# Performance work log

Measured on AMD Instinct MI355X. Metric: run time of the kernel, lower is better.

The kernel has to match this reference:

```python
import jax, jax.numpy as jnp
import numpy as np

D_STATE = 64
D_CONV = 5
HEADDIM = 64
EXPAND = 2


def setup_inputs() -> dict:
    key = jax.random.key(0)
    ks = jax.random.split(key, 12)
    b, ch, h, w = 4, 128, 64, 64
    d_inner = EXPAND * ch
    nheads = d_inner // HEADDIM
    conv_ch = d_inner + 2 * D_STATE
    d_in_proj = 2 * d_inner + 2 * D_STATE + nheads
    s = lambda k, shape, scale: jax.random.normal(k, shape, jnp.float32) * scale
    return {
        "noisy": s(ks[0], (b, ch, h, w), 1.0),
        "aux": s(ks[1], (b, ch, h, w), 1.0),
        "ln_gamma": jnp.ones((ch,), jnp.float32),
        "ln_beta": jnp.zeros((ch,), jnp.float32),
        "in_proj_w": s(ks[2], (d_in_proj, ch), ch ** -0.5),
        "conv_w": s(ks[3], (conv_ch, D_CONV), D_CONV ** -0.5),
        "conv_b": s(ks[4], (conv_ch,), 0.02),
        "A_log": jnp.log(jnp.linspace(1.0, 16.0, nheads)).astype(jnp.float32),
        "dt_bias": s(ks[5], (nheads,), 0.1),
        "D": jnp.ones((nheads,), jnp.float32),
        "rms_w": jnp.ones((d_inner,), jnp.float32),
        "out_proj_w": s(ks[6], (ch, d_inner), d_inner ** -0.5),
        "ff_w1": s(ks[7], (ch, ch, 3, 3), (ch * 9) ** -0.5),
        "ff_b1": jnp.zeros((ch,), jnp.float32),
        "ff_w2": s(ks[8], (ch, ch, 3, 3), (ch * 9) ** -0.5),
        "ff_b2": jnp.zeros((ch,), jnp.float32),
    }


def _mamba2(u, in_proj_w, conv_w, conv_b, A_log, dt_bias, D_skip, rms_w, out_proj_w):
    # u: (b, L, d_model). Mamba2 with ngroups=1, headdim=64.
    b, L, d = u.shape
    d_inner = EXPAND * d
    nheads = d_inner // HEADDIM
    zxbcdt = u @ in_proj_w.T  # (b, L, 2*d_inner + 2*d_state + nheads)
    z = zxbcdt[..., :d_inner]
    xBC = zxbcdt[..., d_inner:2 * d_inner + 2 * D_STATE]
    dt = jax.nn.softplus(zxbcdt[..., -nheads:] + dt_bias)  # (b, L, h)
    # causal depthwise conv1d along L + SiLU
    xBC_c = jnp.transpose(xBC, (0, 2, 1))  # (b, C, L)
    xBC_c = jax.lax.conv_general_dilated(
        xBC_c, conv_w[:, None, :], (1,), [(D_CONV - 1, 0)],
        feature_group_count=xBC_c.shape[1])
    xBC = jax.nn.silu(jnp.transpose(xBC_c + conv_b[None, :, None], (0, 2, 1)))
    x = xBC[..., :d_inner]
    B = xBC[..., d_inner:d_inner + D_STATE]  # (b, L, n)
    C = xBC[..., d_inner + D_STATE:]         # (b, L, n)
    A = -jnp.exp(A_log)                      # (h,)
    xh = x.reshape(b, L, nheads, HEADDIM)    # (b, L, h, p)
    dA = jnp.exp(dt * A)                     # (b, L, h)

    def step(hstate, inputs):
        dA_t, dt_t, x_t, B_t, C_t = inputs
        hstate = hstate * dA_t[:, :, None, None] + jnp.einsum('bh,bhp,bn->bhpn', dt_t, x_t, B_t)
        y_t = jnp.einsum('bhpn,bn->bhp', hstate, C_t)
        return hstate, y_t

    init = jnp.zeros((b, nheads, HEADDIM, D_STATE), u.dtype)
    xs = (jnp.moveaxis(dA, 1, 0), jnp.moveaxis(dt, 1, 0), jnp.moveaxis(xh, 1, 0),
          jnp.moveaxis(B, 1, 0), jnp.moveaxis(C, 1, 0))
    _, ys = jax.lax.scan(step, init, xs)
    y = jnp.moveaxis(ys, 0, 1) + xh * D_skip[None, None, :, None]  # (b, L, h, p)
    y = y.reshape(b, L, d_inner)
    # gated RMSNorm: rmsnorm(y * silu(z)) * weight
    y = y * jax.nn.silu(z)
    y = y * jax.lax.rsqrt(jnp.mean(y * y, axis=-1, keepdims=True) + 1e-5) * rms_w
    return y @ out_proj_w.T


def _conv3x3_reflect(x, w, b):
    x = jnp.pad(x, ((0, 0), (0, 0), (1, 1), (1, 1)), mode='reflect')
    return jax.lax.conv_general_dilated(x, w, (1, 1), 'VALID') + b[None, :, None, None]


def reference(noisy, aux, ln_gamma, ln_beta, in_proj_w, conv_w, conv_b, A_log,
              dt_bias, D, rms_w, out_proj_w, ff_w1, ff_b1, ff_w2, ff_b2):
    b, c, h, w = noisy.shape
    flat = jnp.transpose(noisy, (0, 2, 3, 1)).reshape(b, h * w, c)
    mu = jnp.mean(flat, axis=-1, keepdims=True)
    var = jnp.var(flat, axis=-1, keepdims=True)
    normed = (flat - mu) * jax.lax.rsqrt(var + 1e-5) * ln_gamma + ln_beta
    m = _mamba2(normed, in_proj_w, conv_w, conv_b, A_log, dt_bias, D, rms_w, out_proj_w)
    m = jnp.transpose(m.reshape(b, h, w, c), (0, 3, 1, 2))
    y = noisy + m
    ff = jax.nn.relu(_conv3x3_reflect(y, ff_w1, ff_b1))
    ff = jax.nn.relu(_conv3x3_reflect(ff, ff_w2, ff_b2))
    y = y + ff
    return (y, aux)
```

## Files before the change

kernel.cpp:

```cpp
#include <hip/hip_runtime.h>
#include <cstddef>

#define B_      4
#define C_      128
#define L_      4096
#define DIN     256
#define NH      4
#define HD      64
#define DS      64
#define CONVCH  384
#define DPROJ   644
#define CHUNK   64
#define NCHUNK  64

typedef short bf16x8 __attribute__((ext_vector_type(8)));
typedef float floatx16 __attribute__((ext_vector_type(16)));

__device__ __forceinline__ float siluf(float v) { return v / (1.f + __expf(-v)); }

__device__ __forceinline__ ushort f2bf(float v) {
  unsigned u = __float_as_uint(v);
  unsigned r = (u + 0x7fff + ((u >> 16) & 1)) >> 16;
  return (ushort)r;
}
__device__ __forceinline__ float bf2f(ushort h) {
  return __uint_as_float((unsigned)h << 16);
}

__device__ __forceinline__ void split8(float4 v0, float4 v1, bf16x8& hi, bf16x8& lo) {
  float f[8] = {v0.x, v0.y, v0.z, v0.w, v1.x, v1.y, v1.z, v1.w};
#pragma unroll
  for (int j = 0; j < 8; ++j) {
    ushort h = f2bf(f[j]);
    hi[j] = (short)h;
    lo[j] = (short)f2bf(f[j] - bf2f(h));
  }
}

__global__ __launch_bounds__(256) void wprep_all(
    const float* __restrict__ ipw, ushort* __restrict__ Bh, ushort* __restrict__ Bl,
    const float* __restrict__ opw, ushort* __restrict__ Oh, ushort* __restrict__ Ol,
    const float* __restrict__ fw1, ushort* __restrict__ Wt1,
    const float* __restrict__ fw2, ushort* __restrict__ Wt2) {
  int bi = blockIdx.x;
  int t = threadIdx.x;
  if (bi < 176) {
    int e = bi * 256 + t;
    int d = e >> 6;
    int c0 = (e & 63) * 2;
    int kk = c0 >> 4;
    int l = (d & 31) + 32 * ((c0 & 15) >> 3);
    int j = c0 & 7;
    size_t off = (((size_t)(d >> 5)) * 8 + kk) * 512 + l * 8 + j;
    float v0 = d < 644 ? ipw[(size_t)d * 128 + c0] : 0.f;
    float v1 = d < 644 ? ipw[(size_t)d * 128 + c0 + 1] : 0.f;
    ushort h0 = f2bf(v0), h1 = f2bf(v1);
    *(unsigned*)(Bh + off) = (unsigned)h0 | ((unsigned)h1 << 16);
    *(unsigned*)(Bl + off) = (unsigned)f2bf(v0 - bf2f(h0)) |
                             ((unsigned)f2bf(v1 - bf2f(h1)) << 16);
  } else if (bi < 304) {
    int e = (bi - 176) * 256 + t;
    int d = e >> 8;
    int c = e & 255;
    size_t f = ((size_t)(d >> 5) * 16 + (c >> 4)) * 512 +
               ((d & 31) + 32 * ((c & 15) >> 3)) * 8 + (c & 7);
    float v = opw[(size_t)d * 256 + c];
    ushort h = f2bf(v);
    Oh[f] = h;
    Ol[f] = f2bf(v - bf2f(h));
  } else {
    const float* fw = bi < 432 ? fw1 : fw2;
    ushort* Wt = bi < 432 ? Wt1 : Wt2;
    int co = (bi - 304) & 127;
    int cb = co >> 5;
    for (int e = t; e < 1152; e += 256) {
      int tap = e >> 7;
      int ci = e & 127;
      int kk = ci >> 4, k16 = ci & 15;
      int l = (co & 31) + 32 * (k16 >> 3);
      int off = ((tap * 8 + kk) * 4 + cb) * 512 + l * 8 + (k16 & 7);
      Wt[off] = f2bf(fw[(size_t)co * 1152 + ci * 9 + tap]);
    }
  }
}

__global__ __launch_bounds__(1024) void ln_gemm1(
    const float* __restrict__ noisy, const float* __restrict__ gamma,
    const float* __restrict__ beta,
    const ushort* __restrict__ Bh, const ushort* __restrict__ Bl,
    float* __restrict__ ZX) {
  int row = blockIdx.x, b = blockIdx.y;
  int t = threadIdx.x;
  __shared__ float tile[64 * 129];
  __shared__ float ps[16][64], pq[16][64];
  __shared__ float smu[64], srs[64];
  __shared__ __align__(16) ushort AhL[8192];
  __shared__ __align__(16) ushort AlL[8192];
  int px = t & 63, cg = t >> 6;
  float s = 0.f, s2 = 0.f;
  const float* src = noisy + ((size_t)b * C_) * L_ + row * 64;
  for (int i = 0; i < 8; ++i) {
    int c = cg * 8 + i;
    float v = src[(size_t)c * L_ + px];
    tile[px * 129 + c] = v;
    s += v; s2 += v * v;
  }
  ps[cg][px] = s; pq[cg][px] = s2;
  __syncthreads();
  if (t < 64) {
    float a = 0.f, qq = 0.f;
#pragma unroll
    for (int g = 0; g < 16; ++g) { a += ps[g][t]; qq += pq[g][t]; }
    float mu = a * (1.f / 128.f);
    float var = qq * (1.f / 128.f) - mu * mu;
    smu[t] = mu;
    srs[t] = rsqrtf(var + 1e-5f);
  }
  __syncthreads();
  for (int idx = t; idx < 4096; idx += 1024) {
    int p2 = idx >> 6;
    int c0 = (idx & 63) * 2;
    float v0 = (tile[p2 * 129 + c0] - smu[p2]) * srs[p2] * gamma[c0] + beta[c0];
    float v1 = (tile[p2 * 129 + c0 + 1] - smu[p2]) * srs[p2] * gamma[c0 + 1] + beta[c0 + 1];
    int kk = c0 >> 4;
    int l = (p2 & 31) + 32 * ((c0 & 15) >> 3);
    int j = c0 & 7;
    int off = ((p2 >> 5) * 8 + kk) * 512 + l * 8 + j;
    ushort h0 = f2bf(v0), h1 = f2bf(v1);
    *(unsigned*)(AhL + off) = (unsigned)h0 | ((unsigned)h1 << 16);
    *(unsigned*)(AlL + off) = (unsigned)f2bf(v0 - bf2f(h0)) |
                              ((unsigned)f2bf(v1 - bf2f(h1)) << 16);
  }
  __syncthreads();
  int wv = t >> 6, lane = t & 63;
  int db = wv & 1, pb = (wv >> 1) & 1, bq = wv >> 2;
  int rowadd = 4 * (lane >> 5);
  for (int bn = bq; bn < 11; bn += 4) {
    floatx16 acc;
#pragma unroll
    for (int i = 0; i < 16; ++i) acc[i] = 0.f;
    size_t bbase = ((size_t)(bn * 2 + db) * 8) * 64 + lane;
    const bf16x8* pBh = (const bf16x8*)Bh + bbase;
    const bf16x8* pBl = (const bf16x8*)Bl + bbase;
#pragma unroll
    for (int kk = 0; kk < 8; ++kk) {
      bf16x8 ah = *(const bf16x8*)(AhL + (pb * 8 + kk) * 512 + lane * 8);
      bf16x8 al = *(const bf16x8*)(AlL + (pb * 8 + kk) * 512 + lane * 8);
      bf16x8 bh = pBh[kk * 64];
      bf16x8 bl = pBl[kk * 64];
      acc = __builtin_amdgcn_mfma_f32_32x32x16_bf16(ah, bh, acc, 0, 0, 0);
      acc = __builtin_amdgcn_mfma_f32_32x32x16_bf16(al, bh, acc, 0, 0, 0);
      acc = __builtin_amdgcn_mfma_f32_32x32x16_bf16(ah, bl, acc, 0, 0, 0);
    }
    int d = bn * 64 + db * 32 + (lane & 31);
    if (d < 644) {
#pragma unroll
      for (int r = 0; r < 16; ++r) {
        int rowm = (r & 3) + 8 * (r >> 2) + rowadd;
        int pix = row * 64 + pb * 32 + rowm;
        ZX[((size_t)(b * L_ + pix)) * DPROJ + d] = acc[r];
      }
    }
  }
}

__global__ __launch_bounds__(384) void conv1d_silu(
    const float* __restrict__ ZX, const float* __restrict__ cw,
    const float* __restrict__ cb, float* __restrict__ XBC) {
  int ch = threadIdx.x;
  int l0 = blockIdx.x * 16, b = blockIdx.y;
  const float* base = ZX + ((size_t)b * L_) * DPROJ + DIN + ch;
  float w0 = cw[ch * 5], w1 = cw[ch * 5 + 1], w2 = cw[ch * 5 + 2],
        w3 = cw[ch * 5 + 3], w4 = cw[ch * 5 + 4];
  float bias = cb[ch];
  float win[20];
#pragma unroll
  for (int i = 0; i < 20; ++i) {
    int ll = l0 - 4 + i;
    win[i] = ll >= 0 ? base[(size_t)ll * DPROJ] : 0.f;
  }
  float* dst = XBC + ((size_t)(b * L_ + l0)) * CONVCH + ch;
#pragma unroll
  for (int j = 0; j < 16; ++j) {
    float acc = bias + w0 * win[j] + w1 * win[j + 1] + w2 * win[j + 2] +
                w3 * win[j + 3] + w4 * win[j + 4];
    dst[(size_t)j * CONVCH] = siluf(acc);
  }
}

#define UPDA(k, B4, C4) \
  st[4*k+0] = st[4*k+0]*da + cf*B4.x; y0 += st[4*k+0]*C4.x; \
  st[4*k+1] = st[4*k+1]*da + cf*B4.y; y1 += st[4*k+1]*C4.y; \
  st[4*k+2] = st[4*k+2]*da + cf*B4.z; y2 += st[4*k+2]*C4.z; \
  st[4*k+3] = st[4*k+3]*da + cf*B4.w; y3 += st[4*k+3]*C4.w;

__global__ __launch_bounds__(256, 4) void scan_passA(
    const float* __restrict__ XBC, const float* __restrict__ ZX,
    const float* __restrict__ dt_bias, const float* __restrict__ A_log,
    float* __restrict__ YL, float* __restrict__ SC, float* __restrict__ PC,
    float* __restrict__ CUM) {
  int chunk = blockIdx.x, h = blockIdx.y, b = blockIdx.z;
  int t = threadIdx.x;
  int p = t >> 2, q = t & 3;
  int bh = b * NH + h;
  __shared__ float sdt[CHUNK], sda[CHUNK];
  __shared__ float sB[32][64];
  __shared__ float sCc[32][64];
  __shared__ float sx[32][64];
  if (t < CHUNK) {
    int l = chunk * CHUNK + t;
    float v = ZX[((size_t)(b * L_ + l)) * DPROJ + 640 + h] + dt_bias[h];
    float dt = v > 20.f ? v : log1pf(expf(v));
    sdt[t] = dt;
    sda[t] = expf(dt * -expf(A_log[h]));
  }
  size_t rowbase = ((size_t)b * L_ + (size_t)chunk * CHUNK) * CONVCH;
  float* __restrict__ yl = YL + ((size_t)b * L_ + (size_t)chunk * CHUNK) * DIN + h * HD + p;
  float* __restrict__ cumout = CUM + (size_t)bh * L_ + chunk * CHUNK;
  float st[16];
#pragma unroll
  for (int j = 0; j < 16; ++j) st[j] = 0.f;
  float cum = 1.f;
  for (int half = 0; half < 2; ++half) {
    __syncthreads();
#pragma unroll
    for (int i = 0; i < 2; ++i) {
      int e = t + i * 256;
      int row = e >> 4, c4 = (e & 15) * 4;
      const float* gsrc = XBC + rowbase + (size_t)(half * 32 + row) * CONVCH;
      *(float4*)&sB[row][c4]  = *(const float4*)(gsrc + DIN + c4);
      *(float4*)&sCc[row][c4] = *(const float4*)(gsrc + DIN + DS + c4);
      *(float4*)&sx[row][c4]  = *(const float4*)(gsrc + h * HD + c4);
    }
    __syncthreads();
#pragma unroll 4
    for (int tl = 0; tl < 32; ++tl) {
      int tg = half * 32 + tl;
      float da = sda[tg], dtv = sdt[tg];
      float x = sx[tl][p];
      float cf = dtv * x;
      const float4* br = (const float4*)&sB[tl][q * 16];
      const float4* cr = (const float4*)&sCc[tl][q * 16];
      float4 B0 = br[0], B1 = br[1], B2 = br[2], B3 = br[3];
      float4 C0 = cr[0], C1 = cr[1], C2 = cr[2], C3 = cr[3];
      float y0 = 0.f, y1 = 0.f, y2 = 0.f, y3 = 0.f;
      UPDA(0, B0, C0) UPDA(1, B1, C1) UPDA(2, B2, C2) UPDA(3, B3, C3)
      float y = (y0 + y1) + (y2 + y3);
      y += __shfl_xor(y, 1);
      y += __shfl_xor(y, 2);
      cum *= da;
      if (q == 0) yl[(size_t)tg * DIN] = y;
      if (t == 0) cumout[tg] = cum;
    }
  }
  float* scp = SC + ((size_t)bh * NCHUNK + chunk) * 4096 + p * 64 + q * 16;
  *(float4*)(scp + 0)  = make_float4(st[0], st[1], st[2], st[3]);
  *(float4*)(scp + 4)  = make_float4(st[4], st[5], st[6], st[7]);
  *(float4*)(scp + 8)  = make_float4(st[8], st[9], st[10], st[11]);
  *(float4*)(scp + 12) = make_float4(st[12], st[13], st[14], st[15]);
  if (t == 0) PC[bh * NCHUNK + chunk] = cum;
}

__global__ __launch_bounds__(256) void scan_passB(
    float* __restrict__ SC, const float* __restrict__ PC) {
  int bh = blockIdx.x >> 4;
  int eg = blockIdx.x & 15;
  int e = eg * 256 + threadIdx.x;
  float h = 0.f;
#pragma unroll 8
  for (int c = 0; c < NCHUNK; ++c) {
    size_t idx = ((size_t)bh * NCHUNK + c) * 4096 + e;
    float s = SC[idx];
    float pcv = PC[bh * NCHUNK + c];
    SC[idx] = h;
    h = h * pcv + s;
  }
}

__global__ __launch_bounds__(1024) void passC_gate(
    const float* __restrict__ XBC, const float* __restrict__ SC,
    const float* __restrict__ CUM, const float* __restrict__ Dp,
    const float* __restrict__ YL, const float* __restrict__ ZX,
    const float* __restrict__ rmsw,
    const ushort* __restrict__ Oh, const ushort* __restrict__ Ol,
    const float* __restrict__ noisy, float* __restrict__ YRES) {
  __shared__ float yt[16384];
  __shared__ __align__(16) ushort fr[32768];
  int chunk = blockIdx.x, b = blockIdx.y;
  int t = threadIdx.x;
  int wv = t >> 6, lane = t & 63;
  size_t pix0g = (size_t)b * L_ + (size_t)chunk * CHUNK;
  float* sCcf  = (float*)fr;
  float* scumf = sCcf + 4096;

  float4 zr[4];
  {
    int lp = t & 31, slot2 = t >> 5;
#pragma unroll
    for (int it = 0; it < 2; ++it) {
      const float* z = ZX + (pix0g + it * 32 + slot2) * DPROJ;
      zr[it * 2]     = *(const float4*)(z + lp * 4);
      zr[it * 2 + 1] = *(const float4*)(z + 128 + lp * 4);
    }
  }
  for (int i = t; i < 4096; i += 1024) {
    *(float4*)&yt[i * 4] = *(const float4*)&YL[pix0g * DIN + (size_t)i * 4];
  }
  {
    int px = t >> 4, slot = t & 15;
    float4 cv = *(const float4*)(XBC + (pix0g + px) * CONVCH + DIN + DS + slot * 4);
    ((float4*)sCcf)[px * 16 + (slot ^ (px & 7))] = cv;
    if (t < 256) {
      int hh = t >> 6, px2 = t & 63;
      scumf[t] = CUM[((size_t)(b * NH + hh)) * L_ + chunk * CHUNK + px2];
    }
  }
  __syncthreads();

  {
    int px = t >> 4, c4 = (t & 15) * 4;
    const float* xs = XBC + (pix0g + px) * CONVCH;
#pragma unroll
    for (int hh = 0; hh < 4; ++hh) {
      float4 xv = *(const float4*)(xs + hh * HD + c4);
      float dv = Dp[hh];
      float* dst = &yt[px * 256 + hh * 64 + c4];
      dst[0] += xv.x * dv; dst[1] += xv.y * dv;
      dst[2] += xv.z * dv; dst[3] += xv.w * dv;
    }
  }
  __syncthreads();

  {
    int h1 = wv >> 2, ptile = (wv >> 1) & 1, pxtile = wv & 1;
    int arow = pxtile * 32 + (lane & 31);
    const float* Sb = SC + (((size_t)(b * NH + h1)) * NCHUNK + chunk) * 4096 +
                      (size_t)(ptile * 32 + (lane & 31)) * 64 + (lane >> 5) * 8;
    const float4* av = (const float4*)sCcf + arow * 16;
    int s0 = (lane >> 5) * 2;
    floatx16 acc;
#pragma unroll
    for (int i = 0; i < 16; ++i) acc[i] = 0.f;
#pragma unroll
    for (int kk = 0; kk < 4; ++kk) {
      float4 b0 = *(const float4*)(Sb + kk * 16);
      float4 b1 = *(const float4*)(Sb + kk * 16 + 4);
      int sa = kk * 4 + s0;
      float4 a0 = av[sa ^ (arow & 7)];
      float4 a1 = av[(sa + 1) ^ (arow & 7)];
      bf16x8 ah, al, bh, bl;
      split8(a0, a1, ah, al);
      split8(b0, b1, bh, bl);
      acc = __builtin_amdgcn_mfma_f32_32x32x16_bf16(ah, bh, acc, 0, 0, 0);
      acc = __builtin_amdgcn_mfma_f32_32x32x16_bf16(al, bh, acc, 0, 0, 0);
      acc = __builtin_amdgcn_mfma_f32_32x32x16_bf16(ah, bl, acc, 0, 0, 0);
    }
    int col = h1 * 64 + ptile * 32 + (lane & 31);
    int radd = 4 * (lane >> 5);
#pragma unroll
    for (int r = 0; r < 16; ++r) {
      int pxl = (r & 3) + 8 * (r >> 2) + radd;
      int px = pxtile * 32 + pxl;
      yt[px * 256 + col] += acc[r] * scumf[h1 * 64 + px];
    }
  }
  __syncthreads();

  ushort* AhL = fr;
  ushort* AlL = fr + 16384;
  {
    int lp = t & 31;
    int slot = t >> 5;
    float4 w0 = *(const float4*)(rmsw + lp * 4);
    float4 w1 = *(const float4*)(rmsw + 128 + lp * 4);
#pragma unroll
    for (int it = 0; it < 2; ++it) {
      int pl = it * 32 + slot;
      const float* y = &yt[pl * 256];
      float4 y0 = *(const float4*)(y + lp * 4);
      float4 y1 = *(const float4*)(y + 128 + lp * 4);
      float4 z0 = zr[it * 2];
      float4 z1 = zr[it * 2 + 1];
      float g[8];
      g[0] = y0.x * siluf(z0.x); g[1] = y0.y * siluf(z0.y);
      g[2] = y0.z * siluf(z0.z); g[3] = y0.w * siluf(z0.w);
      g[4] = y1.x * siluf(z1.x); g[5] = y1.y * siluf(z1.y);
      g[6] = y1.z * siluf(z1.z); g[7] = y1.w * siluf(z1.w);
      float ss = 0.f;
#pragma unroll
      for (int j = 0; j < 8; ++j) ss += g[j] * g[j];
      ss += __shfl_xor(ss, 16);
      ss += __shfl_xor(ss, 8);
      ss += __shfl_xor(ss, 4);
      ss += __shfl_xor(ss, 2);
      ss += __shfl_xor(ss, 1);
      float rs = rsqrtf(ss * (1.f / 256.f) + 1e-5f);
      float o[8];
      o[0] = g[0] * rs * w0.x; o[1] = g[1] * rs * w0.y;
      o[2] = g[2] * rs * w0.z; o[3] = g[3] * rs * w0.w;
      o[4] = g[4] * rs * w1.x; o[5] = g[5] * rs * w1.y;
      o[6] = g[6] * rs * w1.z; o[7] = g[7] * rs * w1.w;
#pragma unroll
      for (int grp = 0; grp < 2; ++grp) {
        int d = grp * 128 + lp * 4;
        int off = ((pl >> 5) * 16 + (d >> 4)) * 512 +
                  ((pl & 31) + 32 * ((d & 15) >> 3)) * 8 + (d & 7);
        ushort h0 = f2bf(o[grp*4+0]), h1 = f2bf(o[grp*4+1]);
        ushort h2 = f2bf(o[grp*4+2]), h3 = f2bf(o[grp*4+3]);
        uint2 hv, lv;
        hv.x = (unsigned)h0 | ((unsigned)h1 << 16);
        hv.y = (unsigned)h2 | ((unsigned)h3 << 16);
        lv.x = (unsigned)f2bf(o[grp*4+0] - bf2f(h0)) | ((unsigned)f2bf(o[grp*4+1] - bf2f(h1)) << 16);
        lv.y = (unsigned)f2bf(o[grp*4+2] - bf2f(h2)) | ((unsigned)f2bf(o[grp*4+3] - bf2f(h3)) << 16);
        *(uint2*)(AhL + off) = hv;
        *(uint2*)(AlL + off) = lv;
      }
    }
  }
  __syncthreads();

  floatx16 acc;
#pragma unroll
  for (int i = 0; i < 16; ++i) acc[i] = 0.f;
  int pb = wv >> 2, bn = (wv >> 1) & 1, db = wv & 1;
  int rowadd = 4 * (lane >> 5);
  if (wv < 8) {
    const bf16x8* pBh = (const bf16x8*)Oh;
    const bf16x8* pBl = (const bf16x8*)Ol;
    size_t bbase = ((size_t)(bn * 2 + db) * 16) * 64 + lane;
#pragma unroll
    for (int kk = 0; kk < 16; ++kk) {
      bf16x8 ah = *(const bf16x8*)(AhL + (pb * 16 + kk) * 512 + lane * 8);
      bf16x8 al = *(const bf16x8*)(AlL + (pb * 16 + kk) * 512 + lane * 8);
      bf16x8 bh = pBh[bbase + (size_t)kk * 64];
      bf16x8 bl = pBl[bbase + (size_t)kk * 64];
      acc = __builtin_amdgcn_mfma_f32_32x32x16_bf16(ah, bh, acc, 0, 0, 0);
      acc = __builtin_amdgcn_mfma_f32_32x32x16_bf16(al, bh, acc, 0, 0, 0);
      acc = __builtin_amdgcn_mfma_f32_32x32x16_bf16(ah, bl, acc, 0, 0, 0);
    }
  } else {
    int t2 = t - 512;
#pragma unroll
    for (int k = 0; k < 16; ++k) {
      int idx = t2 + k * 512;
      int c = idx >> 6, px = idx & 63;
      yt[idx] = noisy[((size_t)(b * C_ + c)) * L_ + chunk * CHUNK + px];
    }
  }
  __syncthreads();

  float* tile = (float*)fr;
  if (wv < 8) {
#pragma unroll
    for (int r = 0; r < 16; ++r) {
      int rowm = (r & 3) + 8 * (r >> 2) + rowadd;
      int rowp = pb * 32 + rowm;
      int col = bn * 64 + db * 32 + (lane & 31);
      tile[rowp * 129 + col] = acc[r];
    }
  }
  __syncthreads();
  for (int idx = t; idx < 8192; idx += 1024) {
    int c = idx >> 6, px = idx & 63;
    size_t o = ((size_t)(b * C_ + c)) * L_ + chunk * CHUNK + px;
    YRES[o] = yt[idx] + tile[px * 129 + c];
  }
}

template <int MODE>
__global__ __launch_bounds__(512) void conv3x3_direct(
    const void* __restrict__ inv, const ushort* __restrict__ Wt,
    const float* __restrict__ bias, const float* __restrict__ res,
    void* __restrict__ outv, const float* __restrict__ aux) {
  int y = blockIdx.x, b = blockIdx.y;
  int t = threadIdx.x;
  if (MODE == 1 && blockIdx.z == 1) {
    const float4* s = (const float4*)aux;
    float4* d = (float4*)((float*)outv + 2097152);
    int base = (b * 64 + y) * 512 + t;
#pragma unroll
    for (int k = 0; k < 4; ++k) d[base + k * 131072] = s[base + k * 131072];
    return;
  }
  __shared__ __align__(16) ushort lds[3 * 64 * 128];
  int lane = t & 63;
  int wv = t >> 6;
  int ry[3];
  ry[0] = y == 0 ? 1 : y - 1;
  ry[1] = y;
  ry[2] = y == 63 ? 62 : y + 1;
  {
    int x = lane;
    for (int u = wv; u < 48; u += 8) {
      int r = u / 16;
      int cib = u % 16;
      int ci0 = cib * 8;
      ushort vals[8];
#pragma unroll
      for (int j = 0; j < 8; ++j) {
        size_t src = ((size_t)(b * C_ + ci0 + j)) * L_ + ry[r] * 64 + x;
        if (MODE == 0) vals[j] = f2bf(((const float*)inv)[src]);
        else           vals[j] = ((const ushort*)inv)[src];
      }
      int idx = (r * 64 + x) * 128 + (cib ^ (x & 15)) * 8;
      *(int4*)&lds[idx] = *(int4*)vals;
    }
  }
  __syncthreads();
  int cb = wv >> 1, nb = wv & 1;
  int n = lane & 31, hi = lane >> 5;
  floatx16 acc0, acc1;
#pragma unroll
  for (int i = 0; i < 16; ++i) { acc0[i] = 0.f; acc1[i] = 0.f; }
  const bf16x8* pW = (const bf16x8*)Wt;
  for (int tap = 0; tap < 9; ++tap) {
    int ky = tap / 3, kx = tap % 3;
    int xg = nb * 32 + n + kx - 1;
    int xx = xg < 0 ? 1 : (xg > 63 ? 62 : xg);
    int base = (ky * 64 + xx) * 128;
    int xs = xx & 15;
#pragma unroll
    for (int kk = 0; kk < 8; ++kk) {
      bf16x8 av = pW[(size_t)((tap * 8 + kk) * 4 + cb) * 64 + lane];
      bf16x8 bv = *(const bf16x8*)&lds[base + ((kk * 2 + hi) ^ xs) * 8];
      if (kk & 1) acc1 = __builtin_amdgcn_mfma_f32_32x32x16_bf16(av, bv, acc1, 0, 0, 0);
      else        acc0 = __builtin_amdgcn_mfma_f32_32x32x16_bf16(av, bv, acc0, 0, 0, 0);
    }
  }
  int x0 = nb * 32 + (lane & 31);
  int rowadd = 4 * (lane >> 5);
#pragma unroll
  for (int r = 0; r < 16; ++r) {
    int rowm = (r & 3) + 8 * (r >> 2) + rowadd;
    int co = cb * 32 + rowm;
    size_t o = ((size_t)(b * C_ + co)) * L_ + y * 64 + x0;
    float v = fmaxf(acc0[r] + acc1[r] + bias[co], 0.f);
    if (MODE == 0) {
      ((ushort*)outv)[o] = f2bf(v);
    } else {
      ((float*)outv)[o] = v + res[o];
    }
  }
}

extern "C" void kernel_launch(void* const* d_in, const int* in_sizes, int n_in,
                              void* d_out, int out_size, void* d_ws, size_t ws_size,
                              hipStream_t stream) {
  const float* noisy   = (const float*)d_in[0];
  const float* aux     = (const float*)d_in[1];
  const float* ln_g    = (const float*)d_in[2];
  const float* ln_b    = (const float*)d_in[3];
  const float* ipw     = (const float*)d_in[4];
  const float* cw      = (const float*)d_in[5];
  const float* cbv     = (const float*)d_in[6];
  const float* A_log   = (const float*)d_in[7];
  const float* dt_bias = (const float*)d_in[8];
  const float* Dp      = (const float*)d_in[9];
  const float* rmsw    = (const float*)d_in[10];
  const float* opw     = (const float*)d_in[11];
  const float* fw1     = (const float*)d_in[12];
  const float* fb1     = (const float*)d_in[13];
  const float* fw2     = (const float*)d_in[14];
  const float* fb2     = (const float*)d_in[15];
  float* out = (float*)d_out;
  float* ws  = (float*)d_ws;

  const size_t OFF_ZX   = 0;
  const size_t OFF_XBC  = OFF_ZX + 16384UL * 644;
  const size_t OFF_SCN  = OFF_XBC + 16384UL * 384;
  const size_t OFF_WT   = OFF_SCN + 4194304UL;
  const size_t OFF_WO   = OFF_WT + 73728UL;
  const size_t OFF_CUM  = OFF_WT + 131072UL;
  const size_t OFF_YL   = OFF_CUM + 65536UL;
  const size_t OFF_PC   = OFF_YL + 16384UL * 256;
  const size_t OFF_WT2  = OFF_PC + 1024UL;
  const size_t OFF_YRES = OFF_WT2 + 73728UL;

  float* ZX   = ws + OFF_ZX;
  float* XBC  = ws + OFF_XBC;
  float* SC   = ws + OFF_SCN;
  float* CUM  = ws + OFF_CUM;
  float* YL   = ws + OFF_YL;
  float* PC   = ws + OFF_PC;
  ushort* Bnh  = (ushort*)(ws + OFF_YL);
  ushort* Bnl  = Bnh + 45056UL * 2;
  ushort* Wt1 = (ushort*)(ws + OFF_WT);
  ushort* Woh  = (ushort*)(ws + OFF_WO);
  ushort* Wol  = Woh + 32768UL;
  ushort* Wt2 = (ushort*)(ws + OFF_WT2);
  ushort* FF1 = (ushort*)(ws + OFF_SCN);
  float* YRES = ws + OFF_YRES;

  wprep_all<<<560, 256, 0, stream>>>(ipw, Bnh, Bnl, opw, Woh, Wol, fw1, Wt1, fw2, Wt2);
  ln_gemm1<<<dim3(64, 4), 1024, 0, stream>>>(noisy, ln_g, ln_b, Bnh, Bnl, ZX);
  conv1d_silu<<<dim3(L_ / 16, B_), 384, 0, stream>>>(ZX, cw, cbv, XBC);
  scan_passA<<<dim3(NCHUNK, NH, B_), 256, 0, stream>>>(XBC, ZX, dt_bias, A_log, YL, SC, PC, CUM);
  scan_passB<<<256, 256, 0, stream>>>(SC, PC);
  passC_gate<<<dim3(NCHUNK, B_), 1024, 0, stream>>>(XBC, SC, CUM, Dp, YL, ZX,
                                                    rmsw, Woh, Wol, noisy, YRES);
  conv3x3_direct<0><<<dim3(64, 4), 512, 0, stream>>>(YRES, Wt1, fb1, nullptr, FF1, nullptr);
  conv3x3_direct<1><<<dim3(64, 4, 2), 512, 0, stream>>>(FF1, Wt2, fb2, YRES, out, aux);
}
```

Before: 243.8 us.

## Halve pixel tile per block in ln_gemm1 and passC_gate, doubling grid size

```diff
diff --git a/kernel.cpp b/kernel.cpp
--- a/kernel.cpp
+++ b/kernel.cpp
@@ -84,21 +84,21 @@
   }
 }
 
-__global__ __launch_bounds__(1024) void ln_gemm1(
+__global__ __launch_bounds__(512) void ln_gemm1(
     const float* __restrict__ noisy, const float* __restrict__ gamma,
     const float* __restrict__ beta,
     const ushort* __restrict__ Bh, const ushort* __restrict__ Bl,
     float* __restrict__ ZX) {
   int row = blockIdx.x, b = blockIdx.y;
   int t = threadIdx.x;
-  __shared__ float tile[64 * 129];
-  __shared__ float ps[16][64], pq[16][64];
-  __shared__ float smu[64], srs[64];
-  __shared__ __align__(16) ushort AhL[8192];
-  __shared__ __align__(16) ushort AlL[8192];
-  int px = t & 63, cg = t >> 6;
+  __shared__ float tile[32 * 129];
+  __shared__ float ps[16][32], pq[16][32];
+  __shared__ float smu[32], srs[32];
+  __shared__ __align__(16) ushort AhL[4096];
+  __shared__ __align__(16) ushort AlL[4096];
+  int px = t & 31, cg = t >> 5;
   float s = 0.f, s2 = 0.f;
-  const float* src = noisy + ((size_t)b * C_) * L_ + row * 64;
+  const float* src = noisy + ((size_t)b * C_) * L_ + row * 32;
   for (int i = 0; i < 8; ++i) {
     int c = cg * 8 + i;
     float v = src[(size_t)c * L_ + px];
@@ -107,7 +107,7 @@
   }
   ps[cg][px] = s; pq[cg][px] = s2;
   __syncthreads();
-  if (t < 64) {
+  if (t < 32) {
     float a = 0.f, qq = 0.f;
 #pragma unroll
     for (int g = 0; g < 16; ++g) { a += ps[g][t]; qq += pq[g][t]; }
@@ -117,15 +117,15 @@
     srs[t] = rsqrtf(var + 1e-5f);
   }
   __syncthreads();
-  for (int idx = t; idx < 4096; idx += 1024) {
+  for (int idx = t; idx < 2048; idx += 512) {
     int p2 = idx >> 6;
     int c0 = (idx & 63) * 2;
     float v0 = (tile[p2 * 129 + c0] - smu[p2]) * srs[p2] * gamma[c0] + beta[c0];
     float v1 = (tile[p2 * 129 + c0 + 1] - smu[p2]) * srs[p2] * gamma[c0 + 1] + beta[c0 + 1];
     int kk = c0 >> 4;
-    int l = (p2 & 31) + 32 * ((c0 & 15) >> 3);
+    int l = p2 + 32 * ((c0 & 15) >> 3);
     int j = c0 & 7;
-    int off = ((p2 >> 5) * 8 + kk) * 512 + l * 8 + j;
+    int off = kk * 512 + l * 8 + j;
     ushort h0 = f2bf(v0), h1 = f2bf(v1);
     *(unsigned*)(AhL + off) = (unsigned)h0 | ((unsigned)h1 << 16);
     *(unsigned*)(AlL + off) = (unsigned)f2bf(v0 - bf2f(h0)) |
@@ -133,7 +133,7 @@
   }
   __syncthreads();
   int wv = t >> 6, lane = t & 63;
-  int db = wv & 1, pb = (wv >> 1) & 1, bq = wv >> 2;
+  int db = wv & 1, bq = wv >> 1;
   int rowadd = 4 * (lane >> 5);
   for (int bn = bq; bn < 11; bn += 4) {
     floatx16 acc;
@@ -144,8 +144,8 @@
     const bf16x8* pBl = (const bf16x8*)Bl + bbase;
 #pragma unroll
     for (int kk = 0; kk < 8; ++kk) {
-      bf16x8 ah = *(const bf16x8*)(AhL + (pb * 8 + kk) * 512 + lane * 8);
-      bf16x8 al = *(const bf16x8*)(AlL + (pb * 8 + kk) * 512 + lane * 8);
+      bf16x8 ah = *(const bf16x8*)(AhL + kk * 512 + lane * 8);
+      bf16x8 al = *(const bf16x8*)(AlL + kk * 512 + lane * 8);
       bf16x8 bh = pBh[kk * 64];
       bf16x8 bl = pBl[kk * 64];
       acc = __builtin_amdgcn_mfma_f32_32x32x16_bf16(ah, bh, acc, 0, 0, 0);
@@ -157,7 +157,7 @@
 #pragma unroll
       for (int r = 0; r < 16; ++r) {
         int rowm = (r & 3) + 8 * (r >> 2) + rowadd;
-        int pix = row * 64 + pb * 32 + rowm;
+        int pix = row * 32 + rowm;
         ZX[((size_t)(b * L_ + pix)) * DPROJ + d] = acc[r];
       }
     }
@@ -277,42 +277,44 @@
   }
 }
 
-__global__ __launch_bounds__(1024) void passC_gate(
+__global__ __launch_bounds__(512) void passC_gate(
     const float* __restrict__ XBC, const float* __restrict__ SC,
     const float* __restrict__ CUM, const float* __restrict__ Dp,
     const float* __restrict__ YL, const float* __restrict__ ZX,
     const float* __restrict__ rmsw,
     const ushort* __restrict__ Oh, const ushort* __restrict__ Ol,
     const float* __restrict__ noisy, float* __restrict__ YRES) {
-  __shared__ float yt[16384];
-  __shared__ __align__(16) ushort fr[32768];
-  int chunk = blockIdx.x, b = blockIdx.y;
+  __shared__ float yt[8192];
+  __shared__ __align__(16) ushort fr[16384];
+  int hc = blockIdx.x, b = blockIdx.y;
+  int chunk = hc >> 1;
+  int l0 = hc * 32;
   int t = threadIdx.x;
   int wv = t >> 6, lane = t & 63;
-  size_t pix0g = (size_t)b * L_ + (size_t)chunk * CHUNK;
+  size_t pix0g = (size_t)b * L_ + l0;
   float* sCcf  = (float*)fr;
-  float* scumf = sCcf + 4096;
+  float* scumf = sCcf + 2048;
 
   float4 zr[4];
   {
     int lp = t & 31, slot2 = t >> 5;
 #pragma unroll
     for (int it = 0; it < 2; ++it) {
-      const float* z = ZX + (pix0g + it * 32 + slot2) * DPROJ;
+      const float* z = ZX + (pix0g + it * 16 + slot2) * DPROJ;
       zr[it * 2]     = *(const float4*)(z + lp * 4);
       zr[it * 2 + 1] = *(const float4*)(z + 128 + lp * 4);
     }
   }
-  for (int i = t; i < 4096; i += 1024) {
+  for (int i = t; i < 2048; i += 512) {
     *(float4*)&yt[i * 4] = *(const float4*)&YL[pix0g * DIN + (size_t)i * 4];
   }
   {
     int px = t >> 4, slot = t & 15;
     float4 cv = *(const float4*)(XBC + (pix0g + px) * CONVCH + DIN + DS + slot * 4);
     ((float4*)sCcf)[px * 16 + (slot ^ (px & 7))] = cv;
-    if (t < 256) {
-      int hh = t >> 6, px2 = t & 63;
-      scumf[t] = CUM[((size_t)(b * NH + hh)) * L_ + chunk * CHUNK + px2];
+    if (t < 128) {
+      int hh = t >> 5, px2 = t & 31;
+      scumf[t] = CUM[((size_t)(b * NH + hh)) * L_ + l0 + px2];
     }
   }
   __syncthreads();
@@ -332,8 +334,8 @@
   __syncthreads();
 
   {
-    int h1 = wv >> 2, ptile = (wv >> 1) & 1, pxtile = wv & 1;
-    int arow = pxtile * 32 + (lane & 31);
+    int h1 = wv >> 1, ptile = wv & 1;
+    int arow = lane & 31;
     const float* Sb = SC + (((size_t)(b * NH + h1)) * NCHUNK + chunk) * 4096 +
                       (size_t)(ptile * 32 + (lane & 31)) * 64 + (lane >> 5) * 8;
     const float4* av = (const float4*)sCcf + arow * 16;
@@ -359,15 +361,14 @@
     int radd = 4 * (lane >> 5);
 #pragma unroll
     for (int r = 0; r < 16; ++r) {
-      int pxl = (r & 3) + 8 * (r >> 2) + radd;
-      int px = pxtile * 32 + pxl;
-      yt[px * 256 + col] += acc[r] * scumf[h1 * 64 + px];
+      int px = (r & 3) + 8 * (r >> 2) + radd;
+      yt[px * 256 + col] += acc[r] * scumf[h1 * 32 + px];
     }
   }
   __syncthreads();
 
   ushort* AhL = fr;
-  ushort* AlL = fr + 16384;
+  ushort* AlL = fr + 8192;
   {
     int lp = t & 31;
     int slot = t >> 5;
@@ -375,7 +376,7 @@
     float4 w1 = *(const float4*)(rmsw + 128 + lp * 4);
 #pragma unroll
     for (int it = 0; it < 2; ++it) {
-      int pl = it * 32 + slot;
+      int pl = it * 16 + slot;
       const float* y = &yt[pl * 256];
       float4 y0 = *(const float4*)(y + lp * 4);
       float4 y1 = *(const float4*)(y + 128 + lp * 4);
@@ -403,8 +404,7 @@
 #pragma unroll
       for (int grp = 0; grp < 2; ++grp) {
         int d = grp * 128 + lp * 4;
-        int off = ((pl >> 5) * 16 + (d >> 4)) * 512 +
-                  ((pl & 31) + 32 * ((d & 15) >> 3)) * 8 + (d & 7);
+        int off = (d >> 4) * 512 + (pl + 32 * ((d & 15) >> 3)) * 8 + (d & 7);
         ushort h0 = f2bf(o[grp*4+0]), h1 = f2bf(o[grp*4+1]);
         ushort h2 = f2bf(o[grp*4+2]), h3 = f2bf(o[grp*4+3]);
         uint2 hv, lv;
@@ -422,48 +422,39 @@
   floatx16 acc;
 #pragma unroll
   for (int i = 0; i < 16; ++i) acc[i] = 0.f;
-  int pb = wv >> 2, bn = (wv >> 1) & 1, db = wv & 1;
+  int bn = wv >> 1, db = wv & 1;
   int rowadd = 4 * (lane >> 5);
-  if (wv < 8) {
+  if (wv < 4) {
     const bf16x8* pBh = (const bf16x8*)Oh;
     const bf16x8* pBl = (const bf16x8*)Ol;
     size_t bbase = ((size_t)(bn * 2 + db) * 16) * 64 + lane;
 #pragma unroll
     for (int kk = 0; kk < 16; ++kk) {
-      bf16x8 ah = *(const bf16x8*)(AhL + (pb * 16 + kk) * 512 + lane * 8);
-      bf16x8 al = *(const bf16x8*)(AlL + (pb * 16 + kk) * 512 + lane * 8);
+      bf16x8 ah = *(const bf16x8*)(AhL + kk * 512 + lane * 8);
+      bf16x8 al = *(const bf16x8*)(AlL + kk * 512 + lane * 8);
       bf16x8 bh = pBh[bbase + (size_t)kk * 64];
       bf16x8 bl = pBl[bbase + (size_t)kk * 64];
       acc = __builtin_amdgcn_mfma_f32_32x32x16_bf16(ah, bh, acc, 0, 0, 0);
       acc = __builtin_amdgcn_mfma_f32_32x32x16_bf16(al, bh, acc, 0, 0, 0);
       acc = __builtin_amdgcn_mfma_f32_32x32x16_bf16(ah, bl, acc, 0, 0, 0);
     }
-  } else {
-    int t2 = t - 512;
-#pragma unroll
-    for (int k = 0; k < 16; ++k) {
-      int idx = t2 + k * 512;
-      int c = idx >> 6, px = idx & 63;
-      yt[idx] = noisy[((size_t)(b * C_ + c)) * L_ + chunk * CHUNK + px];
-    }
   }
   __syncthreads();
 
   float* tile = (float*)fr;
-  if (wv < 8) {
+  if (wv < 4) {
 #pragma unroll
     for (int r = 0; r < 16; ++r) {
-      int rowm = (r & 3) + 8 * (r >> 2) + rowadd;
-      int rowp = pb * 32 + rowm;
+      int rowp = (r & 3) + 8 * (r >> 2) + rowadd;
       int col = bn * 64 + db * 32 + (lane & 31);
       tile[rowp * 129 + col] = acc[r];
     }
   }
   __syncthreads();
-  for (int idx = t; idx < 8192; idx += 1024) {
-    int c = idx >> 6, px = idx & 63;
-    size_t o = ((size_t)(b * C_ + c)) * L_ + chunk * CHUNK + px;
-    YRES[o] = yt[idx] + tile[px * 129 + c];
+  for (int idx = t; idx < 4096; idx += 512) {
+    int c = idx >> 5, px = idx & 31;
+    size_t o = ((size_t)(b * C_ + c)) * L_ + l0 + px;
+    YRES[o] = noisy[o] + tile[px * 129 + c];
   }
 }
 
@@ -592,12 +583,12 @@
   float* YRES = ws + OFF_YRES;
 
   wprep_all<<<560, 256, 0, stream>>>(ipw, Bnh, Bnl, opw, Woh, Wol, fw1, Wt1, fw2, Wt2);
-  ln_gemm1<<<dim3(64, 4), 1024, 0, stream>>>(noisy, ln_g, ln_b, Bnh, Bnl, ZX);
+  ln_gemm1<<<dim3(128, 4), 512, 0, stream>>>(noisy, ln_g, ln_b, Bnh, Bnl, ZX);
   conv1d_silu<<<dim3(L_ / 16, B_), 384, 0, stream>>>(ZX, cw, cbv, XBC);
   scan_passA<<<dim3(NCHUNK, NH, B_), 256, 0, stream>>>(XBC, ZX, dt_bias, A_log, YL, SC, PC, CUM);
   scan_passB<<<256, 256, 0, stream>>>(SC, PC);
-  passC_gate<<<dim3(NCHUNK, B_), 1024, 0, stream>>>(XBC, SC, CUM, Dp, YL, ZX,
-                                                    rmsw, Woh, Wol, noisy, YRES);
+  passC_gate<<<dim3(NCHUNK * 2, B_), 512, 0, stream>>>(XBC, SC, CUM, Dp, YL, ZX,
+                                                       rmsw, Woh, Wol, noisy, YRES);
   conv3x3_direct<0><<<dim3(64, 4), 512, 0, stream>>>(YRES, Wt1, fb1, nullptr, FF1, nullptr);
   conv3x3_direct<1><<<dim3(64, 4, 2), 512, 0, stream>>>(FF1, Wt2, fb2, YRES, out, aux);
 }
```

Result: faster. 238.9 us (-2.0%).
